# Kernel optimization log

Measured on AMD Instinct MI355X. Metric: run time of the kernel, lower is better.

Reference implementation:

```python
import jax, jax.numpy as jnp
import numpy as np

KS = 7
DIM = 1024
HEADS = 16
B = 2048

def _rpb_index(ks):
    # Replicates the torch buffer: relative_position_index, shape [ks*ks, ks*ks]
    ch = np.arange(ks)
    coords = np.stack(np.meshgrid(ch, ch, indexing='ij')).reshape(2, -1)  # [2, N]
    rel = coords[:, :, None] - coords[:, None, :]                          # [2, N, N]
    rel = rel.transpose(1, 2, 0).copy()                                    # [N, N, 2]
    rel[:, :, 0] += ks - 1
    rel[:, :, 1] += ks - 1
    rel[:, :, 0] *= 2 * ks - 1
    idx = np.flipud(np.fliplr(rel.sum(-1)))
    return jnp.asarray(idx.copy())

def setup_inputs() -> dict:
    key = jax.random.key(0)
    ks = jax.random.split(key, 4)
    x = jax.random.normal(ks[0], (B, KS, KS, DIM), dtype=jnp.float32)
    qkv_w = jax.random.normal(ks[1], (3 * DIM, DIM), dtype=jnp.float32) * (DIM ** -0.5)
    qkv_b = jnp.zeros((3 * DIM,), dtype=jnp.float32)
    rpb = jax.random.normal(ks[2], (HEADS, 2 * KS - 1, 2 * KS - 1), dtype=jnp.float32) * 0.02
    proj_w = jax.random.normal(ks[3], (DIM, DIM), dtype=jnp.float32) * (DIM ** -0.5)
    proj_b = jnp.zeros((DIM,), dtype=jnp.float32)
    return {"x": x, "qkv_w": qkv_w, "qkv_b": qkv_b, "rpb": rpb, "proj_w": proj_w, "proj_b": proj_b}

def reference(x, qkv_w, qkv_b, rpb, proj_w, proj_b):
    Bn, H, W, C = x.shape
    ksz = H
    N = H * W
    heads = rpb.shape[0]
    hd = C // heads
    scale = hd ** -0.5
    idx = _rpb_index(ksz)  # [N, N] int

    qkv = x.reshape(Bn, N, C) @ qkv_w.T + qkv_b              # [B, N, 3C]
    qkv = qkv.reshape(Bn, N, 3, heads, hd).transpose(2, 0, 3, 1, 4)  # [3, B, h, N, hd]
    q, k, v = qkv[0] * scale, qkv[1], qkv[2]

    attn = jnp.einsum('bhnd,bhmd->bhnm', q, k)               # [B, h, N, N]
    # gather relative-position bias: rpb[h, 2k-1, 2k-1] -> flat [(2k-1)^2, h] -> [N, N, h]
    bias = rpb.transpose(1, 2, 0).reshape(-1, heads)[idx.reshape(-1)]
    bias = bias.reshape(N, N, heads).transpose(2, 0, 1)      # [h, N, N]
    attn = jax.nn.softmax(attn + bias[None], axis=-1)

    out = jnp.einsum('bhnm,bhmd->bhnd', attn, v)             # [B, h, N, hd]
    out = out.transpose(0, 2, 1, 3).reshape(Bn, H, W, C)
    return out @ proj_w.T + proj_b
```

## Files before the change

kernel.cpp:

```cpp
#include <hip/hip_runtime.h>


typedef _Float16 f16;
typedef _Float16 f16x8 __attribute__((ext_vector_type(8)));
typedef _Float16 f16x4 __attribute__((ext_vector_type(4)));
typedef float f32x4 __attribute__((ext_vector_type(4)));

#define G1P(p) ((const __attribute__((address_space(1))) unsigned int*)(p))
#define L3P(p) ((__attribute__((address_space(3))) unsigned int*)(p))

__global__ void cvt_kernel(const float* __restrict__ in, f16* __restrict__ out, int n4) {
  int i = blockIdx.x * blockDim.x + threadIdx.x;
  int stride = gridDim.x * blockDim.x;
  const float4* in4 = (const float4*)in;
  f16x4* out4 = (f16x4*)out;
  for (; i < n4; i += stride) {
    float4 v = in4[i];
    f16x4 o = { (f16)v.x, (f16)v.y, (f16)v.z, (f16)v.w };
    out4[i] = o;
  }
}

__global__ void bias_kernel(const float* __restrict__ rpb, f16* __restrict__ bias_t) {
  int h = blockIdx.x;
  for (int e = threadIdx.x; e < 4096; e += blockDim.x) {
    int m = e >> 6, n = e & 63;
    float v = -60000.f;
    if (n < 49 && m < 49) {
      int in_ = n / 7, jn = n % 7, im = m / 7, jm = m % 7;
      v = rpb[h * 169 + (im - in_ + 6) * 13 + (jm - jn + 6)] * 1.44269504f;
    }
    bias_t[h * 4096 + e] = (f16)v;
  }
}

#define VM4 asm volatile("s_waitcnt vmcnt(4)" ::: "memory")
#define VM0 asm volatile("s_waitcnt vmcnt(0)" ::: "memory")
#define NOVM ((void)0)
#define NOSTG ((void)0)

template <bool HBIN>
__device__ __forceinline__ const f16* aptr(const f16* A, int row, int col, int K) {
  if (HBIN) {
    int bw = row / 49, n = row - bw * 49;
    int h = col >> 6, d = col & 63;
    return A + (size_t)bw * 50176 + h * 3136 + n * 64 + d;
  }
  return A + (size_t)row * K + col;
}

#define STAGEA(ROW0, COL0, LDSOFF)                                                 \
  {                                                                                \
    const f16* s0_ = aptr<HBIN>(A, (ROW0) + wid * 32 + srow, (COL0) + sce, K);     \
    __builtin_amdgcn_global_load_lds(G1P(s0_), L3P(lds + (LDSOFF) + wid * 2048), 16, 0, 0); \
    const f16* s1_ = aptr<HBIN>(A, (ROW0) + wid * 32 + srow + 16, (COL0) + sce, K); \
    __builtin_amdgcn_global_load_lds(G1P(s1_), L3P(lds + (LDSOFF) + wid * 2048 + 1024), 16, 0, 0); \
  }

#define STAGEB(ROW0, COL0, LDSOFF)                                                 \
  {                                                                                \
    const f16* s0_ = B + (size_t)((ROW0) + wid * 32 + srow) * K + ((COL0) + sce);  \
    __builtin_amdgcn_global_load_lds(G1P(s0_), L3P(lds + (LDSOFF) + wid * 2048), 16, 0, 0); \
    const f16* s1_ = s0_ + (size_t)16 * K;                                         \
    __builtin_amdgcn_global_load_lds(G1P(s1_), L3P(lds + (LDSOFF) + wid * 2048 + 1024), 16, 0, 0); \
  }

#define MFMA4(AREG, ROW)                                                           \
  acc[ROW][0] = __builtin_amdgcn_mfma_f32_16x16x32_f16(AREG, b0, acc[ROW][0], 0, 0, 0); \
  acc[ROW][1] = __builtin_amdgcn_mfma_f32_16x16x32_f16(AREG, b1, acc[ROW][1], 0, 0, 0); \
  acc[ROW][2] = __builtin_amdgcn_mfma_f32_16x16x32_f16(AREG, b2, acc[ROW][2], 0, 0, 0); \
  acc[ROW][3] = __builtin_amdgcn_mfma_f32_16x16x32_f16(AREG, b3, acc[ROW][3], 0, 0, 0);

#define PHASE(ABASE, BBASE, MH, STG, VMW)                                          \
  {                                                                                \
    f16x8 a0 = *(const f16x8*)((ABASE) + (wm * 128 + (MH) * 64 +  0 + l15) * 64 + swz); \
    f16x8 a1 = *(const f16x8*)((ABASE) + (wm * 128 + (MH) * 64 + 16 + l15) * 64 + swz); \
    f16x8 a2 = *(const f16x8*)((ABASE) + (wm * 128 + (MH) * 64 + 32 + l15) * 64 + swz); \
    f16x8 a3 = *(const f16x8*)((ABASE) + (wm * 128 + (MH) * 64 + 48 + l15) * 64 + swz); \
    if ((MH) == 0) {                                                               \
      b0 = *(const f16x8*)((BBASE) + (wn * 64 +  0 + l15) * 64 + swz);             \
      b1 = *(const f16x8*)((BBASE) + (wn * 64 + 16 + l15) * 64 + swz);             \
      b2 = *(const f16x8*)((BBASE) + (wn * 64 + 32 + l15) * 64 + swz);             \
      b3 = *(const f16x8*)((BBASE) + (wn * 64 + 48 + l15) * 64 + swz);             \
    }                                                                              \
    STG;                                                                           \
    __builtin_amdgcn_s_barrier();                                                  \
    asm volatile("s_waitcnt lgkmcnt(0)" ::: "memory");                             \
    __builtin_amdgcn_sched_barrier(0);                                             \
    __builtin_amdgcn_s_setprio(1);                                                 \
    MFMA4(a0, (MH) * 4 + 0) MFMA4(a1, (MH) * 4 + 1)                                \
    MFMA4(a2, (MH) * 4 + 2) MFMA4(a3, (MH) * 4 + 3)                                \
    __builtin_amdgcn_s_setprio(0);                                                 \
    VMW;                                                                           \
    __builtin_amdgcn_s_barrier();                                                  \
  }

template <typename OutT, bool HBOUT, bool HBIN>
__global__ __launch_bounds__(512, 2)
void gemm256(const f16* __restrict__ A, const f16* __restrict__ B,
             const float* __restrict__ bias, OutT* __restrict__ C,
             int N, int K, int ntiles_n) {
  __shared__ char lds[131072];
  const int tid = threadIdx.x;
  const int wid = tid >> 6, ln = tid & 63;
  const int l15 = ln & 15, lhi = ln >> 4;
  const int wm = wid >> 2, wn = wid & 3;
  const int srow = ln >> 2;
  const int sce = (((ln & 3) ^ ((ln >> 3) & 3)) << 3);
  const int swz = ((lhi ^ ((l15 >> 1) & 3)) << 4);

  const int nblk = gridDim.x;
  const int wg = (blockIdx.x & 7) * (nblk >> 3) + (blockIdx.x >> 3);
  const int bn = wg % ntiles_n, bm = wg / ntiles_n;
  const int m0 = bm * 256, n0 = bn * 256;

  f32x4 acc[8][4];
#pragma unroll
  for (int i = 0; i < 8; ++i)
#pragma unroll
    for (int j = 0; j < 4; ++j) acc[i][j] = (f32x4){0.f, 0.f, 0.f, 0.f};
  f16x8 b0, b1, b2, b3;

  STAGEA(m0, 0, 0);
  STAGEB(n0, 0, 32768);
  STAGEA(m0, 32, 16384);
  STAGEB(n0, 32, 49152);
  STAGEA(m0, 64, 65536);
  STAGEB(n0, 64, 98304);
  VM4;
  __builtin_amdgcn_s_barrier();

  for (int i = 0; i < 7; ++i) {
    const int cT1k1 = (2 * i + 1) * 64 + 32;
    const int cT2k0 = (2 * i + 2) * 64;
    const int cT2k1 = cT2k0 + 32;
    const int cT3k0 = (2 * i + 3) * 64;
    PHASE(lds + 0,      lds + 32768,  0, STAGEA(m0, cT1k1, 81920),  NOVM);
    PHASE(lds + 0,      lds + 32768,  1, STAGEB(n0, cT1k1, 114688), NOVM);
    PHASE(lds + 16384,  lds + 49152,  0, STAGEA(m0, cT2k0, 0),      NOVM);
    PHASE(lds + 16384,  lds + 49152,  1, STAGEB(n0, cT2k0, 32768),  VM4);
    PHASE(lds + 65536,  lds + 98304,  0, STAGEA(m0, cT2k1, 16384),  NOVM);
    PHASE(lds + 65536,  lds + 98304,  1, STAGEB(n0, cT2k1, 49152),  NOVM);
    PHASE(lds + 81920,  lds + 114688, 0, STAGEA(m0, cT3k0, 65536),  NOVM);
    PHASE(lds + 81920,  lds + 114688, 1, STAGEB(n0, cT3k0, 98304),  VM4);
  }
  PHASE(lds + 0,      lds + 32768,  0, STAGEA(m0, 15 * 64 + 32, 81920),  NOVM);
  PHASE(lds + 0,      lds + 32768,  1, STAGEB(n0, 15 * 64 + 32, 114688), NOVM);
  PHASE(lds + 16384,  lds + 49152,  0, NOSTG, NOVM);
  PHASE(lds + 16384,  lds + 49152,  1, NOSTG, VM0);
  PHASE(lds + 65536,  lds + 98304,  0, NOSTG, NOVM);
  PHASE(lds + 65536,  lds + 98304,  1, NOSTG, NOVM);
  PHASE(lds + 81920,  lds + 114688, 0, NOSTG, NOVM);
  PHASE(lds + 81920,  lds + 114688, 1, NOSTG, NOVM);

  float bv[4];
#pragma unroll
  for (int j = 0; j < 4; ++j) bv[j] = bias[n0 + wn * 64 + j * 16 + l15];
#pragma unroll
  for (int ii = 0; ii < 8; ++ii)
#pragma unroll
    for (int r = 0; r < 4; ++r) {
      int gr = m0 + wm * 128 + ii * 16 + lhi * 4 + r;
      if (HBOUT) {
        int bw = gr / 49, n = gr - bw * 49;
#pragma unroll
        for (int j = 0; j < 4; ++j) {
          int gc = n0 + wn * 64 + j * 16 + l15;
          int which = gc >> 10, rem = gc & 1023;
          int h = rem >> 6, d = rem & 63;
          size_t addr = (((size_t)bw * 16 + h) * 3 + which) * 3136 + n * 64 + d;
          C[addr] = (OutT)(acc[ii][j][r] + bv[j]);
        }
      } else {
#pragma unroll
        for (int j = 0; j < 4; ++j) {
          int gc = n0 + wn * 64 + j * 16 + l15;
          C[(size_t)gr * N + gc] = (OutT)(acc[ii][j][r] + bv[j]);
        }
      }
    }
}

__global__ __launch_bounds__(64)
void attn_kernel(const f16* __restrict__ qkv,
                 const f16* __restrict__ bias_t,
                 f16* __restrict__ out) {
  __shared__ char lds[16384];
  const int bh = blockIdx.x;
  const int h = bh & 15;
  const int ln = threadIdx.x;
  const int l15 = ln & 15, lhi = ln >> 4;
  const size_t qb = (size_t)bh * 3 * 3136;
  const size_t kb = qb + 3136;
  const size_t vb = qb + 6272;

  {
    int rA = ln >> 3, lc = ln & 7;
#pragma unroll
    for (int c = 0; c < 8; ++c) {
      int r = c * 8 + rA;
      int rc = r > 48 ? 48 : r;
      int ce = (lc ^ (r & 7)) << 3;
      const f16* g = qkv + kb + rc * 64 + ce;
      __builtin_amdgcn_global_load_lds(G1P(g), L3P(lds + c * 1024), 16, 0, 0);
    }
  }

  int rv = ln > 48 ? 48 : ln;
  const f16* vp = qkv + vb + rv * 64;
  f16x8 vr[8];
#pragma unroll
  for (int j = 0; j < 8; ++j) vr[j] = *(const f16x8*)(vp + j * 8);

  f16x8 qf[4][2];
#pragma unroll
  for (int t = 0; t < 4; ++t) {
    int rq = t * 16 + l15;
    if (rq > 48) rq = 48;
    const f16* qp = qkv + qb + rq * 64 + lhi * 8;
    qf[t][0] = *(const f16x8*)(qp);
    qf[t][1] = *(const f16x8*)(qp + 32);
  }

  const f16* bb = bias_t + h * 4096;
  f16x4 bq[4][4];
#pragma unroll
  for (int i = 0; i < 4; ++i)
#pragma unroll
    for (int j = 0; j < 4; ++j)
      bq[i][j] = *(const f16x4*)(bb + (j * 16 + l15) * 64 + i * 16 + lhi * 4);

#pragma unroll
  for (int d = 0; d < 64; ++d)
    *(f16*)(lds + 8192 + d * 128 + ((ln * 2) ^ ((d & 7) << 4))) = vr[d >> 3][d & 7];

  asm volatile("s_waitcnt vmcnt(0)" ::: "memory");
  __builtin_amdgcn_sched_barrier(0);

  f32x4 acc[4][4];
#pragma unroll
  for (int i = 0; i < 4; ++i)
#pragma unroll
    for (int j = 0; j < 4; ++j) acc[i][j] = (f32x4){0.f, 0.f, 0.f, 0.f};
#pragma unroll
  for (int kk = 0; kk < 2; ++kk) {
    f16x8 bf[4];
#pragma unroll
    for (int t = 0; t < 4; ++t) {
      int mr = t * 16 + l15;
      int pb = (kk * 64 + lhi * 16) ^ ((mr & 7) << 4);
      bf[t] = *(const f16x8*)(lds + mr * 128 + pb);
    }
    __builtin_amdgcn_s_setprio(1);
#pragma unroll
    for (int i = 0; i < 4; ++i)
#pragma unroll
      for (int j = 0; j < 4; ++j)
        acc[i][j] = __builtin_amdgcn_mfma_f32_16x16x32_f16(qf[i][kk], bf[j], acc[i][j], 0, 0, 0);
    __builtin_amdgcn_s_setprio(0);
  }

  const float SC = 0.125f * 1.44269504f;
#pragma unroll
  for (int i = 0; i < 4; ++i) {
#pragma unroll
    for (int r = 0; r < 4; ++r) {
      int n = i * 16 + lhi * 4 + r;
      float lv[4];
#pragma unroll
      for (int j = 0; j < 4; ++j)
        lv[j] = acc[i][j][r] * SC + (float)bq[i][j][r];
      float Mx = fmaxf(fmaxf(lv[0], lv[1]), fmaxf(lv[2], lv[3]));
#pragma unroll
      for (int off = 1; off < 16; off <<= 1) Mx = fmaxf(Mx, __shfl_xor(Mx, off));
      float s = 0.f;
#pragma unroll
      for (int j = 0; j < 4; ++j) { lv[j] = exp2f(lv[j] - Mx); s += lv[j]; }
#pragma unroll
      for (int off = 1; off < 16; off <<= 1) s += __shfl_xor(s, off);
      float inv = 1.f / s;
#pragma unroll
      for (int j = 0; j < 4; ++j) {
        int m = j * 16 + l15;
        *(f16*)(lds + n * 128 + ((m * 2) ^ ((n & 7) << 4))) = (f16)(lv[j] * inv);
      }
    }
  }

  f32x4 o[4][4];
#pragma unroll
  for (int i = 0; i < 4; ++i)
#pragma unroll
    for (int j = 0; j < 4; ++j) o[i][j] = (f32x4){0.f, 0.f, 0.f, 0.f};
#pragma unroll
  for (int kk = 0; kk < 2; ++kk) {
    f16x8 af[4], bf[4];
#pragma unroll
    for (int t = 0; t < 4; ++t) {
      int nr = t * 16 + l15;
      int pb = (kk * 64 + lhi * 16) ^ ((nr & 7) << 4);
      af[t] = *(const f16x8*)(lds + nr * 128 + pb);
      bf[t] = *(const f16x8*)(lds + 8192 + nr * 128 + pb);
    }
    __builtin_amdgcn_s_setprio(1);
#pragma unroll
    for (int i = 0; i < 4; ++i)
#pragma unroll
      for (int j = 0; j < 4; ++j)
        o[i][j] = __builtin_amdgcn_mfma_f32_16x16x32_f16(af[i], bf[j], o[i][j], 0, 0, 0);
    __builtin_amdgcn_s_setprio(0);
  }
  f16* ob = out + (size_t)bh * 3136;
#pragma unroll
  for (int i = 0; i < 4; ++i)
#pragma unroll
    for (int j = 0; j < 4; ++j)
#pragma unroll
      for (int r = 0; r < 4; ++r) {
        int n = i * 16 + lhi * 4 + r;
        if (n < 49)
          ob[n * 64 + j * 16 + l15] = (f16)o[i][j][r];
      }
}

extern "C" void kernel_launch(void* const* d_in, const int* in_sizes, int n_in,
                              void* d_out, int out_size, void* d_ws, size_t ws_size,
                              hipStream_t stream) {
  const float* x      = (const float*)d_in[0];
  const float* qkv_w  = (const float*)d_in[1];
  const float* qkv_b  = (const float*)d_in[2];
  const float* rpb    = (const float*)d_in[3];
  const float* proj_w = (const float*)d_in[4];
  const float* proj_b = (const float*)d_in[5];
  float* out = (float*)d_out;

  char* ws = (char*)d_ws;
  f16*   x16      = (f16*)(ws);
  f16*   wq16     = (f16*)(ws + 205520896);
  f16*   wp16     = (f16*)(ws + 211812352);
  f16*   qkv16    = (f16*)(ws + 213909504);
  f16*   attnHB   = (f16*)(ws + 830472192);
  f16*   bias_t   = (f16*)(ws + 1035993088);

  cvt_kernel<<<2048, 256, 0, stream>>>(x, x16, 102760448 / 4);
  cvt_kernel<<<1024, 256, 0, stream>>>(qkv_w, wq16, 3145728 / 4);
  cvt_kernel<<<512, 256, 0, stream>>>(proj_w, wp16, 1048576 / 4);
  bias_kernel<<<16, 64, 0, stream>>>(rpb, bias_t);

  gemm256<f16, true, false><<<4704, 512, 0, stream>>>(x16, wq16, qkv_b, qkv16, 3072, 1024, 12);
  attn_kernel<<<2048 * 16, 64, 0, stream>>>(qkv16, bias_t, attnHB);
  gemm256<float, false, true><<<1568, 512, 0, stream>>>(attnHB, wp16, proj_b, out, 1024, 1024, 4);
}
```

Baseline: 1.237 ms.

## Split attention block across two waves and fuse fp32-to-fp16 conversion kernels

The attention kernel now uses two wavefronts per (batch, head) block. Each wave handles 32 query rows: it loads half of K and V into shared memory, synchronises, and writes its own probability tile into a separate LDS region. The aim is to cut per-wave latency and register pressure and to get more parallelism per head, at the cost of two block barriers and some redundant K/V fragment reads. The three conversion launches are also merged into one kernel that branches on index range, removing two launches at the cost of per-element branching.

```diff
diff --git a/kernel.cpp b/kernel.cpp
--- a/kernel.cpp
+++ b/kernel.cpp
@@ -9,15 +9,19 @@
 #define G1P(p) ((const __attribute__((address_space(1))) unsigned int*)(p))
 #define L3P(p) ((__attribute__((address_space(3))) unsigned int*)(p))
 
-__global__ void cvt_kernel(const float* __restrict__ in, f16* __restrict__ out, int n4) {
+__global__ void cvt_all(const float* __restrict__ x, const float* __restrict__ wq,
+                        const float* __restrict__ wp, f16* __restrict__ x16,
+                        f16* __restrict__ wq16, f16* __restrict__ wp16) {
   int i = blockIdx.x * blockDim.x + threadIdx.x;
   int stride = gridDim.x * blockDim.x;
-  const float4* in4 = (const float4*)in;
-  f16x4* out4 = (f16x4*)out;
-  for (; i < n4; i += stride) {
-    float4 v = in4[i];
+  for (; i < 26738688; i += stride) {
+    const float4* src; f16x4* dst; int off;
+    if (i < 25690112) { src = (const float4*)x; dst = (f16x4*)x16; off = i; }
+    else if (i < 26476544) { src = (const float4*)wq; dst = (f16x4*)wq16; off = i - 25690112; }
+    else { src = (const float4*)wp; dst = (f16x4*)wp16; off = i - 26476544; }
+    float4 v = src[off];
     f16x4 o = { (f16)v.x, (f16)v.y, (f16)v.z, (f16)v.w };
-    out4[i] = o;
+    dst[off] = o;
   }
 }
 
@@ -181,23 +185,25 @@
     }
 }
 
-__global__ __launch_bounds__(64)
+__global__ __launch_bounds__(128)
 void attn_kernel(const f16* __restrict__ qkv,
                  const f16* __restrict__ bias_t,
                  f16* __restrict__ out) {
   __shared__ char lds[16384];
   const int bh = blockIdx.x;
   const int h = bh & 15;
-  const int ln = threadIdx.x;
+  const int tid = threadIdx.x;
+  const int w = tid >> 6, ln = tid & 63;
   const int l15 = ln & 15, lhi = ln >> 4;
-  const size_t qb = (size_t)bh * 3 * 3136;
-  const size_t kb = qb + 3136;
-  const size_t vb = qb + 6272;
+  const size_t qb = (size_t)bh * 9408;
+  const size_t kb = qb + 3136, vb = qb + 6272;
+  const int nb = w * 32;
 
   {
     int rA = ln >> 3, lc = ln & 7;
 #pragma unroll
-    for (int c = 0; c < 8; ++c) {
+    for (int cc = 0; cc < 4; ++cc) {
+      int c = w * 4 + cc;
       int r = c * 8 + rA;
       int rc = r > 48 ? 48 : r;
       int ce = (lc ^ (r & 7)) << 3;
@@ -207,15 +213,15 @@
   }
 
   int rv = ln > 48 ? 48 : ln;
-  const f16* vp = qkv + vb + rv * 64;
-  f16x8 vr[8];
-#pragma unroll
-  for (int j = 0; j < 8; ++j) vr[j] = *(const f16x8*)(vp + j * 8);
-
-  f16x8 qf[4][2];
-#pragma unroll
-  for (int t = 0; t < 4; ++t) {
-    int rq = t * 16 + l15;
+  const f16* vp = qkv + vb + rv * 64 + nb;
+  f16x8 vr[4];
+#pragma unroll
+  for (int j = 0; j < 4; ++j) vr[j] = *(const f16x8*)(vp + j * 8);
+
+  f16x8 qf[2][2];
+#pragma unroll
+  for (int t = 0; t < 2; ++t) {
+    int rq = nb + t * 16 + l15;
     if (rq > 48) rq = 48;
     const f16* qp = qkv + qb + rq * 64 + lhi * 8;
     qf[t][0] = *(const f16x8*)(qp);
@@ -223,23 +229,24 @@
   }
 
   const f16* bb = bias_t + h * 4096;
-  f16x4 bq[4][4];
-#pragma unroll
-  for (int i = 0; i < 4; ++i)
+  f16x4 bq[2][4];
+#pragma unroll
+  for (int i = 0; i < 2; ++i)
 #pragma unroll
     for (int j = 0; j < 4; ++j)
-      bq[i][j] = *(const f16x4*)(bb + (j * 16 + l15) * 64 + i * 16 + lhi * 4);
-
-#pragma unroll
-  for (int d = 0; d < 64; ++d)
-    *(f16*)(lds + 8192 + d * 128 + ((ln * 2) ^ ((d & 7) << 4))) = vr[d >> 3][d & 7];
-
-  asm volatile("s_waitcnt vmcnt(0)" ::: "memory");
-  __builtin_amdgcn_sched_barrier(0);
-
-  f32x4 acc[4][4];
-#pragma unroll
-  for (int i = 0; i < 4; ++i)
+      bq[i][j] = *(const f16x4*)(bb + (j * 16 + l15) * 64 + nb + i * 16 + lhi * 4);
+
+#pragma unroll
+  for (int dd = 0; dd < 32; ++dd) {
+    int d = nb + dd;
+    *(f16*)(lds + 8192 + d * 128 + ((ln * 2) ^ ((d & 7) << 4))) = vr[dd >> 3][dd & 7];
+  }
+
+  __syncthreads();
+
+  f32x4 acc[2][4];
+#pragma unroll
+  for (int i = 0; i < 2; ++i)
 #pragma unroll
     for (int j = 0; j < 4; ++j) acc[i][j] = (f32x4){0.f, 0.f, 0.f, 0.f};
 #pragma unroll
@@ -253,19 +260,22 @@
     }
     __builtin_amdgcn_s_setprio(1);
 #pragma unroll
-    for (int i = 0; i < 4; ++i)
+    for (int i = 0; i < 2; ++i)
 #pragma unroll
       for (int j = 0; j < 4; ++j)
         acc[i][j] = __builtin_amdgcn_mfma_f32_16x16x32_f16(qf[i][kk], bf[j], acc[i][j], 0, 0, 0);
     __builtin_amdgcn_s_setprio(0);
   }
 
+  __syncthreads();
+
   const float SC = 0.125f * 1.44269504f;
-#pragma unroll
-  for (int i = 0; i < 4; ++i) {
+  char* pbase = lds + w * 4096;
+#pragma unroll
+  for (int i = 0; i < 2; ++i) {
 #pragma unroll
     for (int r = 0; r < 4; ++r) {
-      int n = i * 16 + lhi * 4 + r;
+      int nl = i * 16 + lhi * 4 + r;
       float lv[4];
 #pragma unroll
       for (int j = 0; j < 4; ++j)
@@ -282,29 +292,32 @@
 #pragma unroll
       for (int j = 0; j < 4; ++j) {
         int m = j * 16 + l15;
-        *(f16*)(lds + n * 128 + ((m * 2) ^ ((n & 7) << 4))) = (f16)(lv[j] * inv);
+        *(f16*)(pbase + nl * 128 + ((m * 2) ^ ((nl & 7) << 4))) = (f16)(lv[j] * inv);
       }
     }
   }
 
-  f32x4 o[4][4];
-#pragma unroll
-  for (int i = 0; i < 4; ++i)
+  f32x4 o[2][4];
+#pragma unroll
+  for (int i = 0; i < 2; ++i)
 #pragma unroll
     for (int j = 0; j < 4; ++j) o[i][j] = (f32x4){0.f, 0.f, 0.f, 0.f};
 #pragma unroll
   for (int kk = 0; kk < 2; ++kk) {
-    f16x8 af[4], bf[4];
-#pragma unroll
-    for (int t = 0; t < 4; ++t) {
-      int nr = t * 16 + l15;
-      int pb = (kk * 64 + lhi * 16) ^ ((nr & 7) << 4);
-      af[t] = *(const f16x8*)(lds + nr * 128 + pb);
-      bf[t] = *(const f16x8*)(lds + 8192 + nr * 128 + pb);
+    f16x8 af[2], bf[4];
+#pragma unroll
+    for (int t = 0; t < 2; ++t) {
+      int nl = t * 16 + l15;
+      af[t] = *(const f16x8*)(pbase + nl * 128 + ((kk * 64 + lhi * 16) ^ ((nl & 7) << 4)));
+    }
+#pragma unroll
+    for (int u = 0; u < 4; ++u) {
+      int dr = u * 16 + l15;
+      bf[u] = *(const f16x8*)(lds + 8192 + dr * 128 + ((kk * 64 + lhi * 16) ^ ((dr & 7) << 4)));
     }
     __builtin_amdgcn_s_setprio(1);
 #pragma unroll
-    for (int i = 0; i < 4; ++i)
+    for (int i = 0; i < 2; ++i)
 #pragma unroll
       for (int j = 0; j < 4; ++j)
         o[i][j] = __builtin_amdgcn_mfma_f32_16x16x32_f16(af[i], bf[j], o[i][j], 0, 0, 0);
@@ -312,12 +325,12 @@
   }
   f16* ob = out + (size_t)bh * 3136;
 #pragma unroll
-  for (int i = 0; i < 4; ++i)
+  for (int i = 0; i < 2; ++i)
 #pragma unroll
     for (int j = 0; j < 4; ++j)
 #pragma unroll
       for (int r = 0; r < 4; ++r) {
-        int n = i * 16 + lhi * 4 + r;
+        int n = nb + i * 16 + lhi * 4 + r;
         if (n < 49)
           ob[n * 64 + j * 16 + l15] = (f16)o[i][j][r];
       }
@@ -342,12 +355,10 @@
   f16*   attnHB   = (f16*)(ws + 830472192);
   f16*   bias_t   = (f16*)(ws + 1035993088);
 
-  cvt_kernel<<<2048, 256, 0, stream>>>(x, x16, 102760448 / 4);
-  cvt_kernel<<<1024, 256, 0, stream>>>(qkv_w, wq16, 3145728 / 4);
-  cvt_kernel<<<512, 256, 0, stream>>>(proj_w, wp16, 1048576 / 4);
+  cvt_all<<<2048, 256, 0, stream>>>(x, qkv_w, proj_w, x16, wq16, wp16);
   bias_kernel<<<16, 64, 0, stream>>>(rpb, bias_t);
 
   gemm256<f16, true, false><<<4704, 512, 0, stream>>>(x16, wq16, qkv_b, qkv16, 3072, 1024, 12);
-  attn_kernel<<<2048 * 16, 64, 0, stream>>>(qkv16, bias_t, attnHB);
+  attn_kernel<<<2048 * 16, 128, 0, stream>>>(qkv16, bias_t, attnHB);
   gemm256<float, false, true><<<1568, 512, 0, stream>>>(attnHB, wp16, proj_b, out, 1024, 1024, 4);
 }
```

After: 1.244 ms. No clear change (+0.6%).
